# Kernel tuning notes

Measured on AMD Instinct MI355X. Metric: run time of the kernel, lower is better.

The kernel has to match this reference:

```python
import jax, jax.numpy as jnp
import numpy as np

DIM = 512
HEAD_DIM = 32
NUM_HEADS = DIM // HEAD_DIM
SCALE = HEAD_DIM ** -0.5
SPARSE_WINDOW = 64
LN_EPS = 1e-5


def setup_inputs() -> dict:
    key = jax.random.key(0)
    ks = jax.random.split(key, 7)
    B, S = 2, 2048
    x = jax.random.normal(ks[0], (B, S, DIM), dtype=jnp.float32)
    # parameters (Linear weights stored as [in, out] for x @ W)
    W_qkv = jax.random.normal(ks[1], (DIM, 2 * DIM), dtype=jnp.float32) * (DIM ** -0.5)
    b_qkv = jnp.zeros((2 * DIM,), dtype=jnp.float32)
    W_out = jax.random.normal(ks[2], (DIM, DIM), dtype=jnp.float32) * (DIM ** -0.5)
    b_out = jnp.zeros((DIM,), dtype=jnp.float32)
    ln_gamma = jnp.ones((DIM,), dtype=jnp.float32)
    ln_beta = jnp.zeros((DIM,), dtype=jnp.float32)
    return {"x": x, "W_qkv": W_qkv, "b_qkv": b_qkv, "W_out": W_out,
            "b_out": b_out, "ln_gamma": ln_gamma, "ln_beta": ln_beta}


def _attn(x, W_qkv, b_qkv, W_out, b_out, ln_gamma, ln_beta):
    B, S, _ = x.shape
    qkv = x @ W_qkv + b_qkv                        # [B,S,2*DIM]
    qk, v = qkv[..., :DIM], qkv[..., DIM:]
    q = jax.nn.silu(qk) * SCALE                    # shared-projection nonlinear Q
    k = jnp.tanh(qk)                               # shared-projection nonlinear K
    q = q.reshape(B, S, NUM_HEADS, HEAD_DIM)
    k = k.reshape(B, S, NUM_HEADS, HEAD_DIM)
    v = v.reshape(B, S, NUM_HEADS, HEAD_DIM)
    scores = jnp.einsum('bihd,bjhd->bhij', q, k)   # [B,H,S,S]
    # sparse window: MULTIPLICATIVE zeroing outside |i-j|<=w (faithful to source)
    i = jnp.arange(S)
    band = (jnp.abs(i[:, None] - i[None, :]) <= SPARSE_WINDOW).astype(scores.dtype)
    scores = scores * band                         # zeros still enter softmax as exp(0)
    probs = jax.nn.softmax(scores, axis=-1)
    out = jnp.einsum('bhij,bjhd->bihd', probs, v).reshape(B, S, DIM)
    out = out @ W_out + b_out
    y = x + out                                    # residual (dropout is eval no-op)
    mu = jnp.mean(y, axis=-1, keepdims=True)
    var = jnp.var(y, axis=-1, keepdims=True)
    return (y - mu) * jax.lax.rsqrt(var + LN_EPS) * ln_gamma + ln_beta


def reference(x, W_qkv, b_qkv, W_out, b_out, ln_gamma, ln_beta):
    return _attn(x, W_qkv, b_qkv, W_out, b_out, ln_gamma, ln_beta)
```

## Files before the change

### kernel.cpp

```cpp
#include <hip/hip_runtime.h>
#include <cstdint>
#include <cstddef>

#define DIMX 512
#define HDIM 32
#define NHEADS 16
#define SEQ 2048
#define BATCH 2
#define MTOT (BATCH*SEQ)
#define WIN 64
#define QSCALE 0.17677669529663687f

typedef __bf16 bf16x8 __attribute__((ext_vector_type(8)));
typedef float f32x4 __attribute__((ext_vector_type(4)));

__device__ __forceinline__ unsigned short f2bf(float f){
  unsigned u = __builtin_bit_cast(unsigned, f);
  u += 0x7FFFu + ((u >> 16) & 1u);
  return (unsigned short)(u >> 16);
}
__device__ __forceinline__ float bf2f(unsigned short s){
  return __builtin_bit_cast(float, ((unsigned)s) << 16);
}
__device__ __forceinline__ unsigned pk(float a, float b){
  return (unsigned)f2bf(a) | ((unsigned)f2bf(b) << 16);
}

__device__ __forceinline__ void gl_lds16(const void* g, void* l){
  __builtin_amdgcn_global_load_lds(
      (const __attribute__((address_space(1))) unsigned*)g,
      (__attribute__((address_space(3))) unsigned*)(unsigned)(unsigned long long)l,
      16, 0, 0);
}

__global__ void k_prep(const float* __restrict__ x, unsigned short* __restrict__ xb,
                       const float* __restrict__ Wq, unsigned short* __restrict__ Wqt,
                       const float* __restrict__ Wo, unsigned short* __restrict__ Wot){
  int bx = blockIdx.x;
  if (bx < 1024){
    int i = bx * 256 + threadIdx.x;
    const float4* p = (const float4*)x + (size_t)i * 2;
    float4 a = p[0], b = p[1];
    uint4 o;
    o.x = pk(a.x, a.y); o.y = pk(a.z, a.w);
    o.z = pk(b.x, b.y); o.w = pk(b.z, b.w);
    ((uint4*)xb)[i] = o;
    return;
  }
  __shared__ float tile[32][33];
  int i = bx - 1024;
  int bxx = i % 48, byy = i / 48;
  const float* W; unsigned short* Wt; int N, n0;
  if (bxx < 32){ W = Wq; Wt = Wqt; N = 1024; n0 = bxx * 32; }
  else         { W = Wo; Wt = Wot; N = 512;  n0 = (bxx - 32) * 32; }
  int k0 = byy * 32;
  int tx = threadIdx.x & 31, ty = threadIdx.x >> 5;
  #pragma unroll
  for (int r = 0; r < 32; r += 8)
    tile[ty + r][tx] = W[(size_t)(k0 + ty + r) * N + n0 + tx];
  __syncthreads();
  #pragma unroll
  for (int r = 0; r < 32; r += 8)
    Wt[(size_t)(n0 + ty + r) * 512 + k0 + tx] = f2bf(tile[tx][ty + r]);
}

template<int MODE, int BM, int NBM, int NBN>
__launch_bounds__(256)
__global__ void k_gemm(const unsigned short* __restrict__ A,
                       const unsigned short* __restrict__ Bt,
                       const float* __restrict__ bias,
                       unsigned short* __restrict__ qb,
                       unsigned short* __restrict__ kb,
                       unsigned short* __restrict__ vt,
                       float* __restrict__ vsum_p,
                       const unsigned short* __restrict__ xb,
                       unsigned short* __restrict__ yb)
{
  const int K = 512;
  constexpr int NWG = NBM * NBN;
  constexpr int MF  = BM / 32;
  __shared__ __align__(16) unsigned short ldsA[2][BM * 64];
  __shared__ __align__(16) unsigned short ldsB[2][64 * 64];
  int tid = threadIdx.x;
  int wid = tid >> 6, lane = tid & 63;
  int wm = wid >> 1, wn = wid & 1;
  int lane15 = lane & 15, laneh = lane >> 4;

  int g = blockIdx.x;
  int gwi = (g & 7) * (NWG / 8) + (g >> 3);
  int bm = gwi / NBN, bn = gwi % NBN;

  f32x4 acc[MF][2] = {};

  int srow_off = lane >> 3;
  int spos     = lane & 7;

  auto STAGE = [&](int buf, int kt){
    int k0 = kt * 64;
    #pragma unroll
    for (int c = 0; c < MF; ++c){
      int cidx = wid * MF + c;
      int r = cidx * 8 + srow_off;
      int ch = spos ^ (r & 7);
      gl_lds16(A + (size_t)(bm * BM + r) * K + k0 + ch * 8, &ldsA[buf][cidx * 512]);
    }
    #pragma unroll
    for (int c = 0; c < 2; ++c){
      int cidx = wid * 2 + c;
      int r = cidx * 8 + srow_off;
      int ch = spos ^ (r & 7);
      gl_lds16(Bt + (size_t)(bn * 64 + r) * K + k0 + ch * 8, &ldsB[buf][cidx * 512]);
    }
  };

  auto COMPUTE = [&](int buf){
    #pragma unroll
    for (int kh = 0; kh < 2; ++kh){
      int chunk = kh * 4 + laneh;
      bf16x8 af[MF], bfv[2];
      #pragma unroll
      for (int mi = 0; mi < MF; ++mi){
        int row = wm * (BM / 2) + mi * 16 + lane15;
        af[mi] = *(const bf16x8*)&ldsA[buf][row * 64 + (chunk ^ (row & 7)) * 8];
      }
      #pragma unroll
      for (int ni = 0; ni < 2; ++ni){
        int row = wn * 32 + ni * 16 + lane15;
        bfv[ni] = *(const bf16x8*)&ldsB[buf][row * 64 + (chunk ^ (row & 7)) * 8];
      }
      #pragma unroll
      for (int mi = 0; mi < MF; ++mi)
        #pragma unroll
        for (int ni = 0; ni < 2; ++ni)
          acc[mi][ni] = __builtin_amdgcn_mfma_f32_16x16x32_bf16(af[mi], bfv[ni], acc[mi][ni], 0, 0, 0);
    }
  };

  STAGE(0, 0);
  __syncthreads();
  #pragma unroll
  for (int kt = 0; kt < 8; ++kt){
    if (kt < 7) STAGE((kt + 1) & 1, kt + 1);
    COMPUTE(kt & 1);
    __syncthreads();
  }

  if (MODE == 0 && bn >= 8){
    unsigned short (*tp)[136] = (unsigned short (*)[136])&ldsA[0][0];
    #pragma unroll
    for (int mi = 0; mi < MF; ++mi)
      #pragma unroll
      for (int ni = 0; ni < 2; ++ni)
        #pragma unroll
        for (int r = 0; r < 4; ++r){
          int ml = wm * (BM / 2) + mi * 16 + laneh * 4 + r;
          int nl = wn * 32 + ni * 16 + lane15;
          tp[nl][ml] = f2bf(acc[mi][ni][r] + bias[bn * 64 + nl]);
        }
    __syncthreads();
    int nl = tid >> 2, q = tid & 3;
    int h = (bn - 8) * 2 + (nl >> 5), d = nl & 31;
    int b = bm >> 4, sc = bm & 15;
    int bh = b * 16 + h;
    uint4 v4[4];
    float ssum = 0.f;
    #pragma unroll
    for (int p = 0; p < 4; ++p){
      v4[p] = *(const uint4*)&tp[nl][q * 32 + p * 8];
      const unsigned* w = (const unsigned*)&v4[p];
      #pragma unroll
      for (int j = 0; j < 4; ++j){
        ssum += bf2f((unsigned short)(w[j] & 0xffff)) + bf2f((unsigned short)(w[j] >> 16));
      }
    }
    ssum += __shfl_xor(ssum, 1); ssum += __shfl_xor(ssum, 2);
    size_t vtoff = (size_t)(bh * HDIM + d) * SEQ + sc * 128 + q * 32;
    #pragma unroll
    for (int p = 0; p < 4; ++p) *(uint4*)(vt + vtoff + p * 8) = v4[p];
    if (q == 0) vsum_p[(sc * 32 + bh) * HDIM + d] = ssum;
  } else {
    #pragma unroll
    for (int mi = 0; mi < MF; ++mi){
      #pragma unroll
      for (int ni = 0; ni < 2; ++ni){
        #pragma unroll
        for (int r = 0; r < 4; ++r){
          int m = bm * BM + wm * (BM / 2) + mi * 16 + laneh * 4 + r;
          int n = bn * 64 + wn * 32 + ni * 16 + lane15;
          float val = acc[mi][ni][r] + bias[n];
          if (MODE == 0){
            float s = val / (1.0f + __expf(-val)) * QSCALE;
            float t = tanhf(val);
            qb[(size_t)m * DIMX + n] = f2bf(s);
            kb[(size_t)m * DIMX + n] = f2bf(t);
          } else {
            size_t idx = (size_t)m * DIMX + n;
            yb[idx] = f2bf(val + bf2f(xb[idx]));
          }
        }
      }
    }
  }
}

__launch_bounds__(256)
__global__ void k_attn(const unsigned short* __restrict__ qb,
                       const unsigned short* __restrict__ kb,
                       const unsigned short* __restrict__ vt,
                       const float* __restrict__ vsum_p,
                       unsigned short* __restrict__ ao)
{
  __shared__ unsigned short p_lds[4][16][40];
  int tid = threadIdx.x, wid = tid >> 6, lane = tid & 63;
  int lane15 = lane & 15, laneh = lane >> 4;
  int bh = blockIdx.y, b = bh >> 4, h = bh & 15;
  int s0 = blockIdx.x * 64 + wid * 16;

  bf16x8 qf = *(const bf16x8*)(qb + (size_t)(b * SEQ + s0 + lane15) * DIMX + h * HDIM + laneh * 8);
  float vs0 = 0.f, vs1 = 0.f;
  #pragma unroll
  for (int c = 0; c < 16; ++c){
    vs0 += vsum_p[(c * 32 + bh) * HDIM + lane15];
    vs1 += vsum_p[(c * 32 + bh) * HDIM + 16 + lane15];
  }

  f32x4 accv[2] = {};
  float dsum[4] = {0.f, 0.f, 0.f, 0.f};

  for (int jt = 0; jt < 9; ++jt){
    int j0 = s0 - 64 + jt * 16;
    int jc = min(max(j0 + lane15, 0), SEQ - 1);
    bf16x8 kf = *(const bf16x8*)(kb + (size_t)(b * SEQ + jc) * DIMX + h * HDIM + laneh * 8);
    f32x4 z = {0.f, 0.f, 0.f, 0.f};
    f32x4 sv = __builtin_amdgcn_mfma_f32_16x16x32_bf16(qf, kf, z, 0, 0, 0);
    #pragma unroll
    for (int r = 0; r < 4; ++r){
      int i = s0 + laneh * 4 + r;
      int j = j0 + lane15;
      int dj = i - j;
      bool inb = (dj <= WIN) && (dj >= -WIN) && (j >= 0) && (j < SEQ);
      float w = inb ? (__expf(sv[r]) - 1.0f) : 0.0f;
      dsum[r] += w;
      p_lds[wid][laneh * 4 + r][(jt & 1) * 16 + lane15] = f2bf(w);
    }
    if (jt & 1){
      int jc0 = j0 - 16;
      bf16x8 pa = *(const bf16x8*)&p_lds[wid][lane15][laneh * 8];
      int jv = min(max(jc0 + laneh * 8, 0), SEQ - 8);
      bf16x8 v0 = *(const bf16x8*)(vt + (size_t)(bh * HDIM + lane15) * SEQ + jv);
      bf16x8 v1 = *(const bf16x8*)(vt + (size_t)(bh * HDIM + 16 + lane15) * SEQ + jv);
      accv[0] = __builtin_amdgcn_mfma_f32_16x16x32_bf16(pa, v0, accv[0], 0, 0, 0);
      accv[1] = __builtin_amdgcn_mfma_f32_16x16x32_bf16(pa, v1, accv[1], 0, 0, 0);
    }
  }
  {
    #pragma unroll
    for (int r = 0; r < 4; ++r)
      p_lds[wid][laneh * 4 + r][16 + lane15] = 0;
    int jc0 = s0 + 64;
    bf16x8 pa = *(const bf16x8*)&p_lds[wid][lane15][laneh * 8];
    int jv = min(max(jc0 + laneh * 8, 0), SEQ - 8);
    bf16x8 v0 = *(const bf16x8*)(vt + (size_t)(bh * HDIM + lane15) * SEQ + jv);
    bf16x8 v1 = *(const bf16x8*)(vt + (size_t)(bh * HDIM + 16 + lane15) * SEQ + jv);
    accv[0] = __builtin_amdgcn_mfma_f32_16x16x32_bf16(pa, v0, accv[0], 0, 0, 0);
    accv[1] = __builtin_amdgcn_mfma_f32_16x16x32_bf16(pa, v1, accv[1], 0, 0, 0);
  }

  #pragma unroll
  for (int r = 0; r < 4; ++r){
    float v = dsum[r];
    v += __shfl_xor(v, 1); v += __shfl_xor(v, 2);
    v += __shfl_xor(v, 4); v += __shfl_xor(v, 8);
    dsum[r] = v;
  }
  #pragma unroll
  for (int r = 0; r < 4; ++r){
    int i = s0 + laneh * 4 + r;
    float dn = (float)SEQ + dsum[r];
    float o0 = (accv[0][r] + vs0) / dn;
    float o1 = (accv[1][r] + vs1) / dn;
    size_t base = (size_t)(b * SEQ + i) * DIMX + h * HDIM;
    ao[base + lane15]      = f2bf(o0);
    ao[base + 16 + lane15] = f2bf(o1);
  }
}

__global__ void k_ln(const unsigned short* __restrict__ yb, const float* __restrict__ gamma,
                     const float* __restrict__ beta, float* __restrict__ out){
  int wid = threadIdx.x >> 6, lane = threadIdx.x & 63;
  int row = blockIdx.x * 4 + wid;
  uint4 u = *(const uint4*)(yb + (size_t)row * DIMX + lane * 8);
  const unsigned* w = (const unsigned*)&u;
  float v[8];
  #pragma unroll
  for (int j = 0; j < 4; ++j){
    v[2*j]   = bf2f((unsigned short)(w[j] & 0xffff));
    v[2*j+1] = bf2f((unsigned short)(w[j] >> 16));
  }
  float s = 0.f, ss = 0.f;
  #pragma unroll
  for (int j = 0; j < 8; ++j){ s += v[j]; ss += v[j] * v[j]; }
  #pragma unroll
  for (int m = 1; m < 64; m <<= 1){ s += __shfl_xor(s, m); ss += __shfl_xor(ss, m); }
  float mu = s * (1.f / DIMX);
  float var = ss * (1.f / DIMX) - mu * mu;
  float inv = rsqrtf(var + 1e-5f);
  float4 g0 = *(const float4*)(gamma + lane * 8);
  float4 g1 = *(const float4*)(gamma + lane * 8 + 4);
  float4 b0 = *(const float4*)(beta + lane * 8);
  float4 b1 = *(const float4*)(beta + lane * 8 + 4);
  float4 o0, o1;
  o0.x = (v[0] - mu) * inv * g0.x + b0.x; o0.y = (v[1] - mu) * inv * g0.y + b0.y;
  o0.z = (v[2] - mu) * inv * g0.z + b0.z; o0.w = (v[3] - mu) * inv * g0.w + b0.w;
  o1.x = (v[4] - mu) * inv * g1.x + b1.x; o1.y = (v[5] - mu) * inv * g1.y + b1.y;
  o1.z = (v[6] - mu) * inv * g1.z + b1.z; o1.w = (v[7] - mu) * inv * g1.w + b1.w;
  float* op = out + (size_t)row * DIMX + lane * 8;
  *(float4*)op = o0; *(float4*)(op + 4) = o1;
}

extern "C" void kernel_launch(void* const* d_in, const int* in_sizes, int n_in,
                              void* d_out, int out_size, void* d_ws, size_t ws_size,
                              hipStream_t stream){
  const float* x      = (const float*)d_in[0];
  const float* W_qkv  = (const float*)d_in[1];
  const float* b_qkv  = (const float*)d_in[2];
  const float* W_out  = (const float*)d_in[3];
  const float* b_out  = (const float*)d_in[4];
  const float* gamma  = (const float*)d_in[5];
  const float* beta   = (const float*)d_in[6];
  float* out = (float*)d_out;

  char* ws = (char*)d_ws;
  size_t off = 0;
  auto alloc = [&](size_t bytes){ void* p = ws + off; off += (bytes + 255) & ~(size_t)255; return p; };
  unsigned short* xb  = (unsigned short*)alloc((size_t)MTOT * DIMX * 2);
  unsigned short* wqt = (unsigned short*)alloc((size_t)1024 * 512 * 2);
  unsigned short* wot = (unsigned short*)alloc((size_t)512 * 512 * 2);
  unsigned short* qb  = (unsigned short*)alloc((size_t)MTOT * DIMX * 2);
  unsigned short* kb  = (unsigned short*)alloc((size_t)MTOT * DIMX * 2);
  unsigned short* vt  = (unsigned short*)alloc((size_t)32 * HDIM * SEQ * 2);
  float*          vsm = (float*)alloc((size_t)16 * 32 * HDIM * 4);
  unsigned short* ao  = (unsigned short*)alloc((size_t)MTOT * DIMX * 2);
  unsigned short* yb  = (unsigned short*)alloc((size_t)MTOT * DIMX * 2);

  k_prep<<<1792, 256, 0, stream>>>(x, xb, W_qkv, wqt, W_out, wot);
  k_gemm<0, 128, 32, 16><<<512, 256, 0, stream>>>(xb, wqt, b_qkv, qb, kb, vt, vsm, nullptr, nullptr);
  k_attn<<<dim3(32, 32), 256, 0, stream>>>(qb, kb, vt, vsm, ao);
  k_gemm<1, 64, 64, 8><<<512, 256, 0, stream>>>(ao, wot, b_out, nullptr, nullptr, nullptr, nullptr, xb, yb);
  k_ln  <<<MTOT / 4, 256, 0, stream>>>(yb, gamma, beta, out);
}
```

Baseline: 48.88 us.

## Enlarge QKV GEMM tile, split-barrier pipeline, head-major Q/K layout, fast tanh

The QKV GEMM tile grows from 128x64 to 128x128 with a unified LDS buffer, so half as many workgroups each reuse more of A. The k-loop replaces __syncthreads with explicit vmcnt waits and raw s_barrier so the prefetch of the next tile overlaps compute. Q and K are now written in a head-major [B,H,S,D] layout so attention reads contiguous 64-byte rows, and tanhf becomes an exp-based formula. Risks: only 256 workgroups, so fewer waves per CU, and the hand-written vmcnt counts must match the number of loads issued.

```diff
diff --git a/kernel.cpp b/kernel.cpp
--- a/kernel.cpp
+++ b/kernel.cpp
@@ -31,6 +31,12 @@
       (const __attribute__((address_space(1))) unsigned*)g,
       (__attribute__((address_space(3))) unsigned*)(unsigned)(unsigned long long)l,
       16, 0, 0);
+}
+
+template<int N> __device__ __forceinline__ void vmwait(){
+  if      constexpr (N ==  8) asm volatile("s_waitcnt vmcnt(8)"  ::: "memory");
+  else if constexpr (N ==  4) asm volatile("s_waitcnt vmcnt(4)"  ::: "memory");
+  else                        asm volatile("s_waitcnt vmcnt(0)"  ::: "memory");
 }
 
 __global__ void k_prep(const float* __restrict__ x, unsigned short* __restrict__ xb,
@@ -64,7 +70,7 @@
     Wt[(size_t)(n0 + ty + r) * 512 + k0 + tx] = f2bf(tile[tx][ty + r]);
 }
 
-template<int MODE, int BM, int NBM, int NBN>
+template<int MODE, int BM, int BN, int NBN>
 __launch_bounds__(256)
 __global__ void k_gemm(const unsigned short* __restrict__ A,
                        const unsigned short* __restrict__ Bt,
@@ -77,10 +83,10 @@
                        unsigned short* __restrict__ yb)
 {
   const int K = 512;
-  constexpr int NWG = NBM * NBN;
-  constexpr int MF  = BM / 32;
-  __shared__ __align__(16) unsigned short ldsA[2][BM * 64];
-  __shared__ __align__(16) unsigned short ldsB[2][64 * 64];
+  constexpr int NWG = (MTOT / BM) * NBN;
+  constexpr int MF  = BM / 32, NF = BN / 32;
+  constexpr int LPS = (BM + BN) / 32;
+  __shared__ __align__(16) unsigned short lds[2][(BM + BN) * 64];
   int tid = threadIdx.x;
   int wid = tid >> 6, lane = tid & 63;
   int wm = wid >> 1, wn = wid & 1;
@@ -90,7 +96,7 @@
   int gwi = (g & 7) * (NWG / 8) + (g >> 3);
   int bm = gwi / NBN, bn = gwi % NBN;
 
-  f32x4 acc[MF][2] = {};
+  f32x4 acc[MF][NF] = {};
 
   int srow_off = lane >> 3;
   int spos     = lane & 7;
@@ -102,14 +108,14 @@
       int cidx = wid * MF + c;
       int r = cidx * 8 + srow_off;
       int ch = spos ^ (r & 7);
-      gl_lds16(A + (size_t)(bm * BM + r) * K + k0 + ch * 8, &ldsA[buf][cidx * 512]);
-    }
-    #pragma unroll
-    for (int c = 0; c < 2; ++c){
-      int cidx = wid * 2 + c;
+      gl_lds16(A + (size_t)(bm * BM + r) * K + k0 + ch * 8, &lds[buf][cidx * 512]);
+    }
+    #pragma unroll
+    for (int c = 0; c < NF; ++c){
+      int cidx = wid * NF + c;
       int r = cidx * 8 + srow_off;
       int ch = spos ^ (r & 7);
-      gl_lds16(Bt + (size_t)(bn * 64 + r) * K + k0 + ch * 8, &ldsB[buf][cidx * 512]);
+      gl_lds16(Bt + (size_t)(bn * BN + r) * K + k0 + ch * 8, &lds[buf][BM * 64 + cidx * 512]);
     }
   };
 
@@ -117,82 +123,88 @@
     #pragma unroll
     for (int kh = 0; kh < 2; ++kh){
       int chunk = kh * 4 + laneh;
-      bf16x8 af[MF], bfv[2];
+      bf16x8 af[MF], bfv[NF];
       #pragma unroll
       for (int mi = 0; mi < MF; ++mi){
         int row = wm * (BM / 2) + mi * 16 + lane15;
-        af[mi] = *(const bf16x8*)&ldsA[buf][row * 64 + (chunk ^ (row & 7)) * 8];
+        af[mi] = *(const bf16x8*)&lds[buf][row * 64 + (chunk ^ (row & 7)) * 8];
       }
       #pragma unroll
-      for (int ni = 0; ni < 2; ++ni){
-        int row = wn * 32 + ni * 16 + lane15;
-        bfv[ni] = *(const bf16x8*)&ldsB[buf][row * 64 + (chunk ^ (row & 7)) * 8];
+      for (int ni = 0; ni < NF; ++ni){
+        int row = wn * (BN / 2) + ni * 16 + lane15;
+        bfv[ni] = *(const bf16x8*)&lds[buf][BM * 64 + row * 64 + (chunk ^ (row & 7)) * 8];
       }
       #pragma unroll
       for (int mi = 0; mi < MF; ++mi)
         #pragma unroll
-        for (int ni = 0; ni < 2; ++ni)
+        for (int ni = 0; ni < NF; ++ni)
           acc[mi][ni] = __builtin_amdgcn_mfma_f32_16x16x32_bf16(af[mi], bfv[ni], acc[mi][ni], 0, 0, 0);
     }
   };
 
   STAGE(0, 0);
-  __syncthreads();
   #pragma unroll
   for (int kt = 0; kt < 8; ++kt){
     if (kt < 7) STAGE((kt + 1) & 1, kt + 1);
+    if (kt < 7) vmwait<LPS>(); else vmwait<0>();
+    __builtin_amdgcn_s_barrier();
+    __builtin_amdgcn_sched_barrier(0);
     COMPUTE(kt & 1);
-    __syncthreads();
-  }
-
-  if (MODE == 0 && bn >= 8){
-    unsigned short (*tp)[136] = (unsigned short (*)[136])&ldsA[0][0];
+    __builtin_amdgcn_s_barrier();
+    __builtin_amdgcn_sched_barrier(0);
+  }
+
+  if (MODE == 0 && bn >= 4){
+    unsigned short (*tp)[136] = (unsigned short (*)[136])&lds[0][0];
     #pragma unroll
     for (int mi = 0; mi < MF; ++mi)
       #pragma unroll
-      for (int ni = 0; ni < 2; ++ni)
+      for (int ni = 0; ni < NF; ++ni)
         #pragma unroll
         for (int r = 0; r < 4; ++r){
           int ml = wm * (BM / 2) + mi * 16 + laneh * 4 + r;
-          int nl = wn * 32 + ni * 16 + lane15;
-          tp[nl][ml] = f2bf(acc[mi][ni][r] + bias[bn * 64 + nl]);
+          int nl = wn * (BN / 2) + ni * 16 + lane15;
+          tp[nl][ml] = f2bf(acc[mi][ni][r] + bias[bn * BN + nl]);
         }
     __syncthreads();
-    int nl = tid >> 2, q = tid & 3;
-    int h = (bn - 8) * 2 + (nl >> 5), d = nl & 31;
+    int nl = tid >> 1, half = tid & 1;
+    int h = (bn - 4) * 4 + (nl >> 5), d = nl & 31;
     int b = bm >> 4, sc = bm & 15;
     int bh = b * 16 + h;
-    uint4 v4[4];
+    uint4 v4[8];
     float ssum = 0.f;
     #pragma unroll
-    for (int p = 0; p < 4; ++p){
-      v4[p] = *(const uint4*)&tp[nl][q * 32 + p * 8];
+    for (int p = 0; p < 8; ++p){
+      v4[p] = *(const uint4*)&tp[nl][half * 64 + p * 8];
       const unsigned* w = (const unsigned*)&v4[p];
       #pragma unroll
-      for (int j = 0; j < 4; ++j){
+      for (int j = 0; j < 4; ++j)
         ssum += bf2f((unsigned short)(w[j] & 0xffff)) + bf2f((unsigned short)(w[j] >> 16));
-      }
-    }
-    ssum += __shfl_xor(ssum, 1); ssum += __shfl_xor(ssum, 2);
-    size_t vtoff = (size_t)(bh * HDIM + d) * SEQ + sc * 128 + q * 32;
-    #pragma unroll
-    for (int p = 0; p < 4; ++p) *(uint4*)(vt + vtoff + p * 8) = v4[p];
-    if (q == 0) vsum_p[(sc * 32 + bh) * HDIM + d] = ssum;
+    }
+    ssum += __shfl_xor(ssum, 1);
+    size_t vtoff = (size_t)(bh * HDIM + d) * SEQ + sc * 128 + half * 64;
+    #pragma unroll
+    for (int p = 0; p < 8; ++p) *(uint4*)(vt + vtoff + p * 8) = v4[p];
+    if (half == 0) vsum_p[(sc * 32 + bh) * HDIM + d] = ssum;
   } else {
     #pragma unroll
     for (int mi = 0; mi < MF; ++mi){
       #pragma unroll
-      for (int ni = 0; ni < 2; ++ni){
+      for (int ni = 0; ni < NF; ++ni){
         #pragma unroll
         for (int r = 0; r < 4; ++r){
           int m = bm * BM + wm * (BM / 2) + mi * 16 + laneh * 4 + r;
-          int n = bn * 64 + wn * 32 + ni * 16 + lane15;
+          int nloc = wn * (BN / 2) + ni * 16 + lane15;
+          int n = bn * BN + nloc;
           float val = acc[mi][ni][r] + bias[n];
           if (MODE == 0){
-            float s = val / (1.0f + __expf(-val)) * QSCALE;
-            float t = tanhf(val);
-            qb[(size_t)m * DIMX + n] = f2bf(s);
-            kb[(size_t)m * DIMX + n] = f2bf(t);
+            int b = m >> 11, s = m & 2047;
+            int h = n >> 5, d = n & 31;
+            size_t idx = ((size_t)(b * 16 + h) * SEQ + s) * HDIM + d;
+            float sv = val / (1.0f + __expf(-val)) * QSCALE;
+            float tv = 1.0f - 2.0f / (1.0f + __expf(2.0f * val));
+            qb[idx] = f2bf(sv);
+            kb[idx] = f2bf(tv);
           } else {
             size_t idx = (size_t)m * DIMX + n;
             yb[idx] = f2bf(val + bf2f(xb[idx]));
@@ -216,7 +228,7 @@
   int bh = blockIdx.y, b = bh >> 4, h = bh & 15;
   int s0 = blockIdx.x * 64 + wid * 16;
 
-  bf16x8 qf = *(const bf16x8*)(qb + (size_t)(b * SEQ + s0 + lane15) * DIMX + h * HDIM + laneh * 8);
+  bf16x8 qf = *(const bf16x8*)(qb + ((size_t)bh * SEQ + s0 + lane15) * HDIM + laneh * 8);
   float vs0 = 0.f, vs1 = 0.f;
   #pragma unroll
   for (int c = 0; c < 16; ++c){
@@ -230,7 +242,7 @@
   for (int jt = 0; jt < 9; ++jt){
     int j0 = s0 - 64 + jt * 16;
     int jc = min(max(j0 + lane15, 0), SEQ - 1);
-    bf16x8 kf = *(const bf16x8*)(kb + (size_t)(b * SEQ + jc) * DIMX + h * HDIM + laneh * 8);
+    bf16x8 kf = *(const bf16x8*)(kb + ((size_t)bh * SEQ + jc) * HDIM + laneh * 8);
     f32x4 z = {0.f, 0.f, 0.f, 0.f};
     f32x4 sv = __builtin_amdgcn_mfma_f32_16x16x32_bf16(qf, kf, z, 0, 0, 0);
     #pragma unroll
@@ -344,7 +356,7 @@
   unsigned short* yb  = (unsigned short*)alloc((size_t)MTOT * DIMX * 2);
 
   k_prep<<<1792, 256, 0, stream>>>(x, xb, W_qkv, wqt, W_out, wot);
-  k_gemm<0, 128, 32, 16><<<512, 256, 0, stream>>>(xb, wqt, b_qkv, qb, kb, vt, vsm, nullptr, nullptr);
+  k_gemm<0, 128, 128, 8><<<256, 256, 0, stream>>>(xb, wqt, b_qkv, qb, kb, vt, vsm, nullptr, nullptr);
   k_attn<<<dim3(32, 32), 256, 0, stream>>>(qb, kb, vt, vsm, ao);
   k_gemm<1, 64, 64, 8><<<512, 256, 0, stream>>>(ao, wot, b_out, nullptr, nullptr, nullptr, nullptr, xb, yb);
   k_ln  <<<MTOT / 4, 256, 0, stream>>>(yb, gamma, beta, out);
```

Result: faster. 45.03 us (-7.9%).
